# Performance work log

Hardware: AMD Instinct MI355X
Metric: run time of the kernel (lower is better)

## Reference

```python
import jax, jax.numpy as jnp
import numpy as np

B, N, IN, E, H, F = 64, 256, 128, 256, 8, 1024


def setup_inputs() -> dict:
    key = jax.random.key(0)
    ks = jax.random.split(key, 16)
    x = jax.random.normal(ks[0], (B, N, IN), jnp.float32)
    adj = (jax.random.uniform(ks[1], (B, N, N)) < 0.1).astype(jnp.float32)
    adj = jnp.maximum(adj, adj.transpose(0, 2, 1))  # symmetric 0/1 adjacency
    mask = jax.random.randint(ks[2], (B, N), 0, 2).astype(jnp.float32)
    dist = jax.random.normal(ks[3], (B, N, N), jnp.float32)

    def lin(k, i, o):
        return (jax.random.normal(k, (i, o), jnp.float32) / np.sqrt(i)).astype(jnp.float32)

    return dict(
        x=x, adj=adj, mask=mask, dist=dist,
        W1=lin(ks[4], IN, E), b1=jnp.zeros((E,), jnp.float32),
        W2=lin(ks[5], E, E), b2=jnp.zeros((E,), jnp.float32),
        W3=lin(ks[6], E, E), b3=jnp.zeros((E,), jnp.float32),
        ln1_g=jnp.ones((E,), jnp.float32), ln1_b=jnp.zeros((E,), jnp.float32),
        Wq=lin(ks[7], E, H * E), Wk=lin(ks[8], E, H * E), Wv=lin(ks[9], E, H * E),
        Wo=lin(ks[10], H * E, E), bo=jnp.zeros((E,), jnp.float32),
        ln2_g=jnp.ones((E,), jnp.float32), ln2_b=jnp.zeros((E,), jnp.float32),
        Wf1=lin(ks[11], E, F), bf1=jnp.zeros((F,), jnp.float32),
        Wf2=lin(ks[12], F, E), bf2=jnp.zeros((E,), jnp.float32),
    )


def _layernorm(x, g, b):
    m = x.mean(-1, keepdims=True)
    v = ((x - m) ** 2).mean(-1, keepdims=True)
    return (x - m) * jax.lax.rsqrt(v + 1e-5) * g + b


def reference(x, adj, mask, dist, W1, b1, W2, b2, W3, b3, ln1_g, ln1_b,
              Wq, Wk, Wv, Wo, bo, ln2_g, ln2_b, Wf1, bf1, Wf2, bf2):
    # --- DenseGCNConv normalization (add self-loops, sym-normalize) ---
    eye = jnp.eye(N, dtype=adj.dtype)
    A = adj * (1.0 - eye) + eye                      # fill_diag(adj, 1)
    dis = jax.lax.rsqrt(jnp.clip(A.sum(-1), 1.0, None))
    An = dis[:, :, None] * A * dis[:, None, :]       # D^-1/2 A D^-1/2, [B,N,N]
    m3 = mask[:, :, None]

    def gcn(h, W, b):
        return (jnp.einsum('bij,bjf->bif', An, h @ W) + b) * m3

    g1 = jax.nn.relu(gcn(x, W1, b1))
    g2 = jax.nn.relu(gcn(g1, W2, b2))
    g3 = jax.nn.relu(gcn(g2, W3, b3))
    gcn_res = g1 + g2 + g3

    # --- masked MHA with distance bias (head dim = E per head) ---
    h = _layernorm(gcn_res, ln1_g, ln1_b)
    mh = mask[:, None, :, None]                      # [B,1,N,1]
    q = (h @ Wq).reshape(B, N, H, E).transpose(0, 2, 1, 3) * mh
    k = (h @ Wk).reshape(B, N, H, E).transpose(0, 2, 1, 3) * mh
    v = (h @ Wv).reshape(B, N, H, E).transpose(0, 2, 1, 3) * mh
    a = jnp.einsum('bhne,bhme->bhnm', q * (E ** -0.5), k) + dist[:, None]
    am = (mask[:, :, None] * mask[:, None, :])[:, None]  # [B,1,N,N]
    a = jnp.where(am == 0, -1e9, a)
    a = jax.nn.softmax(a, axis=-1)
    a = jnp.where(am == 0, 0.0, a)
    y = jnp.einsum('bhnm,bhme->bhne', a, v).transpose(0, 2, 1, 3).reshape(B, N, H * E)
    y = (y @ Wo + bo) * m3
    att = gcn_res + y

    # --- FFN block ---
    f = _layernorm(att, ln2_g, ln2_b)
    f = (jax.nn.gelu(f @ Wf1 + bf1, approximate=False) @ Wf2 + bf2) * m3
    att = att + f
    return gcn_res + att
```

## Files before the change

### kernel.cpp

```cpp
#include <hip/hip_runtime.h>
#include <hip/hip_bf16.h>
#include <cmath>

#define BB 64
#define NNODES 256
#define INF_ 128
#define EE 256
#define HH 8
#define FFN 1024
#define BNROWS 16384

typedef __attribute__((ext_vector_type(8))) short short8;
typedef __attribute__((ext_vector_type(4))) float floatx4;
typedef __attribute__((ext_vector_type(4))) unsigned short ushort4v;

__device__ __forceinline__ float b2f(unsigned short u) {
  union { unsigned u32; float f; } w; w.u32 = ((unsigned)u) << 16; return w.f;
}
__device__ __forceinline__ unsigned short f2b(float f) {
  union { float f; unsigned u32; } w; w.f = f;
  unsigned r = w.u32 + 0x7FFFu + ((w.u32 >> 16) & 1u);
  return (unsigned short)(r >> 16);
}
__device__ __forceinline__ float gelu_f(float x) {
  const float z = 0.7978845608028654f * (x + 0.044715f * x * x * x);
  const float e = __expf(2.0f * z);
  const float th = (e - 1.0f) / (e + 1.0f);
  return 0.5f * x * (1.0f + th);
}

typedef const __attribute__((address_space(1))) void GV;
typedef __attribute__((address_space(3))) void LV;

__device__ __forceinline__ void gl_lds16(const unsigned short* g,
                                         unsigned short* l, int lane) {
#if __has_builtin(__builtin_amdgcn_global_load_lds)
  __builtin_amdgcn_global_load_lds((GV*)g, (LV*)l, 16, 0, 0);
#else
  *(short8*)(l + lane * 8) = *(const short8*)g;
#endif
}

struct PackArgs {
  const float* src[10];
  unsigned short* dst[10];
  int R[10], C[10];
  int start[11];
};

__launch_bounds__(256)
__global__ void pack_kernel(PackArgs a)
{
  __shared__ float tile[32][33];
  const int bid = blockIdx.x;
  int j = 0;
  while (bid >= a.start[j + 1]) j++;
  const int lb = bid - a.start[j];
  const float* src = a.src[j];
  unsigned short* dst = a.dst[j];
  const int R = a.R[j], C = a.C[j];

  if (C == 0) {
    const int i = (lb * 256 + threadIdx.x) * 4;
    if (i >= R) return;
    floatx4 v = *(const floatx4*)(src + i);
    ushort4v o;
    #pragma unroll
    for (int k = 0; k < 4; k++) o[k] = f2b(v[k]);
    *(ushort4v*)(dst + i) = o;
    return;
  }
  const int tpr = C >> 5;
  const int c0 = (lb % tpr) * 32, r0 = (lb / tpr) * 32;
  const int tx = threadIdx.x & 31, ty = threadIdx.x >> 5;
  #pragma unroll
  for (int i = ty; i < 32; i += 8)
    tile[i][tx] = src[(long long)(r0 + i) * C + c0 + tx];
  __syncthreads();
  #pragma unroll
  for (int i = ty; i < 32; i += 8)
    dst[(long long)(c0 + i) * R + r0 + tx] = f2b(tile[tx][i]);
}

__launch_bounds__(1024)
__global__ void an_kernel(const float* __restrict__ adj,
                          unsigned short* __restrict__ An)
{
  __shared__ float dis[256];
  const int b = blockIdx.x;
  const float* A = adj + (long long)b * 65536;
  const int t = threadIdx.x;
  const int row = t >> 2, seg = t & 3;
  const float* p = A + row * 256 + seg * 64;
  float s = 0.f;
  for (int k = 0; k < 64; k += 4) {
    floatx4 v = *(const floatx4*)(p + k);
    #pragma unroll
    for (int jj = 0; jj < 4; jj++) {
      const int col = seg * 64 + k + jj;
      s += (col == row) ? 1.0f : v[jj];
    }
  }
  s += __shfl_xor(s, 1);
  s += __shfl_xor(s, 2);
  if (seg == 0) dis[row] = 1.0f / sqrtf(fmaxf(s, 1.0f));
  __syncthreads();
  const float di = dis[row];
  unsigned short* dst = An + (long long)b * 65536 + row * 256 + seg * 64;
  for (int k = 0; k < 64; k += 4) {
    floatx4 v = *(const floatx4*)(p + k);
    ushort4v o;
    #pragma unroll
    for (int jj = 0; jj < 4; jj++) {
      const int col = seg * 64 + k + jj;
      o[jj] = f2b(di * dis[col] * ((col == row) ? 1.0f : v[jj]));
    }
    *(ushort4v*)(dst + k) = o;
  }
}

__launch_bounds__(512, 4)
__global__ void gemm_kernel(const unsigned short* __restrict__ A, int lda,
                            long long sAo, long long sAi,
                            const unsigned short* __restrict__ Bm, int ldb,
                            long long sBo, long long sBi,
                            void* __restrict__ Cv, int ldc,
                            long long sCo, long long sCi,
                            int K, int zshift, int mode, int flag,
                            const float* __restrict__ aux1,
                            const float* __restrict__ mask,
                            float* __restrict__ gcn,
                            void* __restrict__ aux2)
{
  __shared__ __align__(16) unsigned short sA[16384];
  __shared__ __align__(16) unsigned short sB[16384];

  const int t = threadIdx.x;
  const int z = blockIdx.z;
  const int zi = z & ((1 << zshift) - 1);
  const int zb = z >> zshift;
  const int m0 = blockIdx.x * 128;
  const int n0 = blockIdx.y * 128;
  A  += zb * sAo + zi * sAi;
  Bm += zb * sBo + zi * sBi;
  const long long cbase = zb * sCo + zi * sCi;

  const int lane = t & 63;
  const int w = t >> 6;
  const int wm = w >> 2, wn = w & 3;
  const int lm = lane & 15, qd = lane >> 4;

  floatx4 acc[4][2] = {};

  const int sub = lane >> 4;
  const int qs  = lane & 15;
  const unsigned short* pA[4];
  const unsigned short* pB[4];
  #pragma unroll
  for (int i = 0; i < 4; i++) {
    const int d = w * 4 + i;
    const int r = d * 4 + sub;
    const int co = (qs ^ (r & 7)) * 8;
    pA[i] = A + (long long)(m0 + r) * lda + co;
    pB[i] = Bm + (long long)(n0 + r) * ldb + co;
  }

  for (int kk = 0; kk < K; kk += 128) {
    #pragma unroll
    for (int i = 0; i < 4; i++) {
      gl_lds16(pA[i] + kk, &sA[(w * 4 + i) * 512], lane);
      gl_lds16(pB[i] + kk, &sB[(w * 4 + i) * 512], lane);
    }
    __syncthreads();

    #pragma unroll
    for (int ks = 0; ks < 4; ks++) {
      short8 af[4], bg[2];
      const int q = ks * 4 + qd;
      #pragma unroll
      for (int mi = 0; mi < 4; mi++) {
        const int r = wm * 64 + mi * 16 + lm;
        af[mi] = *(const short8*)&sA[r * 128 + ((q ^ (r & 7)) * 8)];
      }
      #pragma unroll
      for (int ni = 0; ni < 2; ni++) {
        const int r = wn * 32 + ni * 16 + lm;
        bg[ni] = *(const short8*)&sB[r * 128 + ((q ^ (r & 7)) * 8)];
      }
      #pragma unroll
      for (int mi = 0; mi < 4; mi++)
        #pragma unroll
        for (int ni = 0; ni < 2; ni++)
          acc[mi][ni] = __builtin_amdgcn_mfma_f32_16x16x32_bf16(
              af[mi], bg[ni], acc[mi][ni], 0, 0, 0);
    }
    __syncthreads();
  }

  #pragma unroll
  for (int mi = 0; mi < 4; mi++) {
    const int row0 = m0 + wm * 64 + mi * 16 + qd * 4;
    #pragma unroll
    for (int ni = 0; ni < 2; ni++) {
      const int col = n0 + wn * 32 + ni * 16 + lm;
      floatx4 a = acc[mi][ni];
      if (mode == 0) {
        float* Cf = (float*)Cv;
        #pragma unroll
        for (int r = 0; r < 4; r++)
          Cf[cbase + (long long)(row0 + r) * ldc + col] = a[r];
      } else if (mode == 1) {
        unsigned short* Cb = (unsigned short*)Cv;
        #pragma unroll
        for (int r = 0; r < 4; r++)
          Cb[cbase + (long long)(row0 + r) * ldc + col] = f2b(a[r]);
      } else if (mode == 2) {
        float* Cf = (float*)Cv;
        #pragma unroll
        for (int r = 0; r < 4; r++)
          Cf[cbase + (long long)(row0 + r) * ldc + col] += a[r];
      } else if (mode == 3) {
        unsigned short* Cb = (unsigned short*)Cv;
        const float bv = aux1[col];
        #pragma unroll
        for (int r = 0; r < 4; r++)
          Cb[cbase + (long long)(row0 + r) * ldc + col] = f2b(gelu_f(a[r] + bv));
      } else if (mode == 5) {
        const int b = row0 >> 8, n = row0 & 255;
        ushort4v o;
        #pragma unroll
        for (int r = 0; r < 4; r++) o[r] = f2b(a[r]);
        *(ushort4v*)((unsigned short*)Cv + (long long)b * 65536 + col * 256 + n) = o;
      } else if (mode == 8) {
        float* Cf = (float*)Cv;
        const float* attf = (const float*)aux2;
        const float bv = aux1[col];
        #pragma unroll
        for (int r = 0; r < 4; r++) {
          const long long idx = (long long)(row0 + r) * 256 + col;
          Cf[idx] = gcn[idx] + attf[idx] + (a[r] + bv) * mask[row0 + r];
        }
      } else if (mode == 9) {
        const int token = zb * 256 + col;
        const float m = mask[token];
        ushort4v o; floatx4 g;
        #pragma unroll
        for (int r = 0; r < 4; r++) {
          const float v = fmaxf((a[r] + aux1[row0 + r]) * m, 0.f);
          o[r] = f2b(v); g[r] = v;
        }
        *(ushort4v*)((unsigned short*)Cv + (long long)token * 256 + row0) = o;
        float* gp = gcn + (long long)token * 256 + row0;
        if (flag) { floatx4 old = *(const floatx4*)gp; g += old; }
        *(floatx4*)gp = g;
      } else if (mode == 12) {
        float* Cf = (float*)Cv;
        const float bv = aux1[col];
        #pragma unroll
        for (int r = 0; r < 4; r++) {
          const long long idx = (long long)(row0 + r) * 256 + col;
          Cf[idx] = gcn[idx] + (a[r] + bv) * mask[row0 + r];
        }
      } else if (mode == 13) {
        unsigned short* Cb = (unsigned short*)Cv;
        #pragma unroll
        for (int r = 0; r < 4; r++)
          Cb[cbase + (long long)(row0 + r) * ldc + col] = f2b(a[r] * 0.0625f);
      } else {
        const int z2 = (row0 >> 8) * 8 + (col >> 8);
        const int e = col & 255, n = row0 & 255;
        ushort4v o;
        #pragma unroll
        for (int r = 0; r < 4; r++) o[r] = f2b(a[r]);
        *(ushort4v*)((unsigned short*)Cv + (long long)z2 * 65536 + e * 256 + n) = o;
      }
    }
  }
}

__launch_bounds__(512, 2)
__global__ void attn_kernel(const unsigned short* __restrict__ HBF,
                            const unsigned short* __restrict__ ABH,
                            const unsigned short* __restrict__ VT,
                            unsigned short* __restrict__ YB,
                            const float* __restrict__ dist,
                            const float* __restrict__ mask)
{
  __shared__ __align__(16) unsigned short sA8[8192];
  __shared__ __align__(16) unsigned short sB16[16384];
  __shared__ float redm[4][128];
  __shared__ float reds[4][128];

  const int mt = blockIdx.x;
  const int z  = blockIdx.y;
  const int b  = z >> 3, h = z & 7;
  const int t = threadIdx.x, lane = t & 63, w = t >> 6;
  const int wm = w >> 2, wn = w & 3;
  const int lm = lane & 15, qd = lane >> 4;
  const int m0 = mt * 128;

  const unsigned short* Hm = HBF + ((long long)(b * 256 + m0)) * 256;
  const unsigned short* Hb = HBF + ((long long)(b * 256)) * 256;
  const unsigned short* AB = ABH + (long long)h * 65536;
  const unsigned short* Vb = VT + (long long)z * 65536;
  unsigned short* Yb = YB + ((long long)(b * 256 + m0)) * 2048 + h * 256;
  const float* maskb = mask + b * 256;
  const float* distb = dist + (long long)b * 65536;

  const int rin = lane >> 3;
  const int qs  = lane & 7;

  floatx4 T[4][4] = {};
  for (int c = 0; c < 4; c++) {
    const int e0 = c * 64;
    #pragma unroll
    for (int i = 0; i < 2; i++) {
      const int d = w * 2 + i;
      const int r = d * 8 + rin;
      gl_lds16(Hm + (long long)r * 256 + e0 + ((qs ^ (r & 7)) * 8),
               &sA8[d * 512], lane);
    }
    #pragma unroll
    for (int i = 0; i < 4; i++) {
      const int d = w * 4 + i;
      const int r = d * 8 + rin;
      gl_lds16(AB + (long long)r * 256 + e0 + ((qs ^ (r & 7)) * 8),
               &sB16[d * 512], lane);
    }
    __syncthreads();
    #pragma unroll
    for (int ks = 0; ks < 2; ks++) {
      short8 af[4], bg4[4];
      const int o = ks * 4 + qd;
      #pragma unroll
      for (int mi = 0; mi < 4; mi++) {
        const int r = wm * 64 + mi * 16 + lm;
        af[mi] = *(const short8*)&sA8[r * 64 + ((o ^ (r & 7)) * 8)];
      }
      #pragma unroll
      for (int ni = 0; ni < 4; ni++) {
        const int r = wn * 64 + ni * 16 + lm;
        bg4[ni] = *(const short8*)&sB16[r * 64 + ((o ^ (r & 7)) * 8)];
      }
      #pragma unroll
      for (int mi = 0; mi < 4; mi++)
        #pragma unroll
        for (int ni = 0; ni < 4; ni++)
          T[mi][ni] = __builtin_amdgcn_mfma_f32_16x16x32_bf16(
              af[mi], bg4[ni], T[mi][ni], 0, 0, 0);
    }
    __syncthreads();
  }

  floatx4 S[4][4] = {};
  for (int c = 0; c < 4; c++) {
    #pragma unroll
    for (int i = 0; i < 4; i++) {
      const int d = w * 4 + i;
      const int r = d * 8 + rin;
      gl_lds16(Hb + (long long)r * 256 + c * 64 + ((qs ^ (r & 7)) * 8),
               &sB16[d * 512], lane);
    }
    if (wn == c) {
      #pragma unroll
      for (int mi = 0; mi < 4; mi++)
        #pragma unroll
        for (int r = 0; r < 4; r++) {
          const int row = wm * 64 + mi * 16 + qd * 4 + r;
          #pragma unroll
          for (int ni = 0; ni < 4; ni++) {
            const int kl = ni * 16 + lm;
            const int slot = (kl >> 3) ^ (row & 7);
            sA8[row * 64 + slot * 8 + (kl & 7)] = f2b(T[mi][ni][r]);
          }
        }
    }
    __syncthreads();
    #pragma unroll
    for (int ks = 0; ks < 2; ks++) {
      short8 af[4], bg4[4];
      const int o = ks * 4 + qd;
      #pragma unroll
      for (int mi = 0; mi < 4; mi++) {
        const int r = wm * 64 + mi * 16 + lm;
        af[mi] = *(const short8*)&sA8[r * 64 + ((o ^ (r & 7)) * 8)];
      }
      #pragma unroll
      for (int ni = 0; ni < 4; ni++) {
        const int r = wn * 64 + ni * 16 + lm;
        bg4[ni] = *(const short8*)&sB16[r * 64 + ((o ^ (r & 7)) * 8)];
      }
      #pragma unroll
      for (int mi = 0; mi < 4; mi++)
        #pragma unroll
        for (int ni = 0; ni < 4; ni++)
          S[mi][ni] = __builtin_amdgcn_mfma_f32_16x16x32_bf16(
              af[mi], bg4[ni], S[mi][ni], 0, 0, 0);
    }
    __syncthreads();
  }

  #pragma unroll
  for (int i = 0; i < 4; i++) {
    const int d = w * 4 + i;
    const int r = d * 8 + rin;
    gl_lds16(Vb + (long long)r * 256 + ((qs ^ (r & 7)) * 8),
             &sB16[d * 512], lane);
  }

  float mk[4];
  #pragma unroll
  for (int ni = 0; ni < 4; ni++) mk[ni] = maskb[wn * 64 + ni * 16 + lm];

  float lred[4][4];
  #pragma unroll
  for (int mi = 0; mi < 4; mi++) {
    #pragma unroll
    for (int r = 0; r < 4; r++) {
      const int row = wm * 64 + mi * 16 + qd * 4 + r;
      const float mq = maskb[m0 + row];
      float mx = -3e38f;
      #pragma unroll
      for (int ni = 0; ni < 4; ni++) {
        const int col = wn * 64 + ni * 16 + lm;
        const float dv = distb[(long long)(m0 + row) * 256 + col];
        const float v = (mq != 0.f && mk[ni] != 0.f) ? (S[mi][ni][r] + dv) : -1e9f;
        S[mi][ni][r] = v;
        mx = fmaxf(mx, v);
      }
      lred[mi][r] = mx;
    }
  }
  #pragma unroll
  for (int off = 1; off < 16; off <<= 1)
    #pragma unroll
    for (int mi = 0; mi < 4; mi++)
      #pragma unroll
      for (int r = 0; r < 4; r++)
        lred[mi][r] = fmaxf(lred[mi][r], __shfl_xor(lred[mi][r], off));
  if (lm == 0)
    #pragma unroll
    for (int mi = 0; mi < 4; mi++)
      #pragma unroll
      for (int r = 0; r < 4; r++)
        redm[wn][wm * 64 + mi * 16 + qd * 4 + r] = lred[mi][r];
  __syncthreads();

  #pragma unroll
  for (int mi = 0; mi < 4; mi++) {
    #pragma unroll
    for (int r = 0; r < 4; r++) {
      const int row = wm * 64 + mi * 16 + qd * 4 + r;
      const float gmax = fmaxf(fmaxf(redm[0][row], redm[1][row]),
                               fmaxf(redm[2][row], redm[3][row]));
      float s = 0.f;
      #pragma unroll
      for (int ni = 0; ni < 4; ni++) {
        const float e = __expf(S[mi][ni][r] - gmax);
        S[mi][ni][r] = e;
        s += e;
      }
      lred[mi][r] = s;
    }
  }
  #pragma unroll
  for (int off = 1; off < 16; off <<= 1)
    #pragma unroll
    for (int mi = 0; mi < 4; mi++)
      #pragma unroll
      for (int r = 0; r < 4; r++)
        lred[mi][r] += __shfl_xor(lred[mi][r], off);
  if (lm == 0)
    #pragma unroll
    for (int mi = 0; mi < 4; mi++)
      #pragma unroll
      for (int r = 0; r < 4; r++)
        reds[wn][wm * 64 + mi * 16 + qd * 4 + r] = lred[mi][r];
  __syncthreads();

  #pragma unroll
  for (int mi = 0; mi < 4; mi++) {
    #pragma unroll
    for (int r = 0; r < 4; r++) {
      const int row = wm * 64 + mi * 16 + qd * 4 + r;
      const float gs = reds[0][row] + reds[1][row] + reds[2][row] + reds[3][row];
      const float inv = 1.0f / gs;
      #pragma unroll
      for (int ni = 0; ni < 4; ni++) S[mi][ni][r] *= inv;
    }
  }

  floatx4 Y[4][4] = {};
  for (int c = 0; c < 4; c++) {
    if (wn == c) {
      #pragma unroll
      for (int mi = 0; mi < 4; mi++)
        #pragma unroll
        for (int r = 0; r < 4; r++) {
          const int row = wm * 64 + mi * 16 + qd * 4 + r;
          #pragma unroll
          for (int ni = 0; ni < 4; ni++) {
            const int kl = ni * 16 + lm;
            const int slot = (kl >> 3) ^ (row & 7);
            sA8[row * 64 + slot * 8 + (kl & 7)] = f2b(S[mi][ni][r]);
          }
        }
    }
    __syncthreads();
    #pragma unroll
    for (int ks = 0; ks < 2; ks++) {
      short8 af[4], bg4[4];
      const int o = ks * 4 + qd;
      #pragma unroll
      for (int mi = 0; mi < 4; mi++) {
        const int r = wm * 64 + mi * 16 + lm;
        af[mi] = *(const short8*)&sA8[r * 64 + ((o ^ (r & 7)) * 8)];
      }
      #pragma unroll
      for (int ni = 0; ni < 4; ni++) {
        const int r = wn * 64 + ni * 16 + lm;
        bg4[ni] = *(const short8*)&sB16[r * 64 + ((o ^ (r & 7)) * 8)];
      }
      #pragma unroll
      for (int mi = 0; mi < 4; mi++)
        #pragma unroll
        for (int ni = 0; ni < 4; ni++)
          Y[mi][ni] = __builtin_amdgcn_mfma_f32_16x16x32_bf16(
              af[mi], bg4[ni], Y[mi][ni], 0, 0, 0);
    }
    __syncthreads();
    if (c < 3) {
      #pragma unroll
      for (int i = 0; i < 4; i++) {
        const int d = w * 4 + i;
        const int r = d * 8 + rin;
        gl_lds16(Vb + (long long)r * 256 + (c + 1) * 64 + ((qs ^ (r & 7)) * 8),
                 &sB16[d * 512], lane);
      }
    }
  }

  #pragma unroll
  for (int mi = 0; mi < 4; mi++)
    #pragma unroll
    for (int ni = 0; ni < 4; ni++) {
      const int col = wn * 64 + ni * 16 + lm;
      #pragma unroll
      for (int r = 0; r < 4; r++) {
        const int row = wm * 64 + mi * 16 + qd * 4 + r;
        Yb[(long long)row * 2048 + col] = f2b(Y[mi][ni][r]);
      }
    }
}

__global__ void ln_kernel(const float* __restrict__ X,
                          const float* __restrict__ gam,
                          const float* __restrict__ bet,
                          unsigned short* __restrict__ out)
{
  const int g = blockIdx.x * 4 + (threadIdx.x >> 6);
  const int lane = threadIdx.x & 63;
  floatx4 v = *(const floatx4*)(X + (long long)g * 256 + lane * 4);
  float s = v[0] + v[1] + v[2] + v[3];
  float sq = v[0]*v[0] + v[1]*v[1] + v[2]*v[2] + v[3]*v[3];
  #pragma unroll
  for (int off = 32; off > 0; off >>= 1) {
    s  += __shfl_xor(s, off);
    sq += __shfl_xor(sq, off);
  }
  const float mean = s * (1.0f / 256.0f);
  const float var = sq * (1.0f / 256.0f) - mean * mean;
  const float rs = 1.0f / sqrtf(var + 1e-5f);
  ushort4v o;
  #pragma unroll
  for (int jj = 0; jj < 4; jj++) {
    const int c = lane * 4 + jj;
    o[jj] = f2b((v[jj] - mean) * rs * gam[c] + bet[c]);
  }
  *(ushort4v*)(out + (long long)g * 256 + lane * 4) = o;
}

static inline void launch_gemm(hipStream_t st, int M, int N, int batch,
    const void* A, int lda, long long sAo, long long sAi,
    const void* B, int ldb, long long sBo, long long sBi,
    void* C, int ldc, long long sCo, long long sCi,
    int K, int zshift, int mode, int flag,
    const float* aux1, const float* mask, float* gcn, void* aux2)
{
  dim3 grid(M / 128, N / 128, batch), blk(512);
  gemm_kernel<<<grid, blk, 0, st>>>(
      (const unsigned short*)A, lda, sAo, sAi,
      (const unsigned short*)B, ldb, sBo, sBi,
      C, ldc, sCo, sCi, K, zshift, mode, flag, aux1, mask, gcn, aux2);
}

extern "C" void kernel_launch(void* const* d_in, const int* in_sizes, int n_in,
                              void* d_out, int out_size, void* d_ws, size_t ws_size,
                              hipStream_t stream)
{
  (void)in_sizes; (void)n_in; (void)out_size;
  const float* x    = (const float*)d_in[0];
  const float* adj  = (const float*)d_in[1];
  const float* mask = (const float*)d_in[2];
  const float* dist = (const float*)d_in[3];
  const float* W1   = (const float*)d_in[4];
  const float* b1   = (const float*)d_in[5];
  const float* W2   = (const float*)d_in[6];
  const float* b2   = (const float*)d_in[7];
  const float* W3   = (const float*)d_in[8];
  const float* b3   = (const float*)d_in[9];
  const float* ln1g = (const float*)d_in[10];
  const float* ln1b = (const float*)d_in[11];
  const float* Wq   = (const float*)d_in[12];
  const float* Wk   = (const float*)d_in[13];
  const float* Wv   = (const float*)d_in[14];
  const float* Wo   = (const float*)d_in[15];
  const float* bo   = (const float*)d_in[16];
  const float* ln2g = (const float*)d_in[17];
  const float* ln2b = (const float*)d_in[18];
  const float* Wf1  = (const float*)d_in[19];
  const float* bf1  = (const float*)d_in[20];
  const float* Wf2  = (const float*)d_in[21];
  const float* bf2  = (const float*)d_in[22];

  char* w = (char*)d_ws;
  auto alloc = [&](size_t sz) { void* p = (void*)w; w += sz; return p; };
  unsigned short* W1T   = (unsigned short*)alloc(65536);
  unsigned short* W2T   = (unsigned short*)alloc(131072);
  unsigned short* W3T   = (unsigned short*)alloc(131072);
  unsigned short* WVT   = (unsigned short*)alloc(1048576);
  unsigned short* WOT   = (unsigned short*)alloc(1048576);
  unsigned short* WF1T  = (unsigned short*)alloc(524288);
  unsigned short* WF2T  = (unsigned short*)alloc(524288);
  unsigned short* WQb   = (unsigned short*)alloc(1048576);
  unsigned short* WKb   = (unsigned short*)alloc(1048576);
  unsigned short* ABH   = (unsigned short*)alloc(1048576);
  unsigned short* XBF   = (unsigned short*)alloc(4194304);
  float*          GCN   = (float*)         alloc(16777216);
  float*          U     = (float*)         alloc(16777216);
  unsigned short* HBF   = (unsigned short*)alloc(8388608);
  char* scratch = (char*)alloc(134217728);
  if ((size_t)(w - (char*)d_ws) > ws_size) return;
  unsigned short* AN  = (unsigned short*)scratch;
  unsigned short* TT  = (unsigned short*)(scratch + 8388608);
  unsigned short* GBF = (unsigned short*)(scratch + 16777216);
  unsigned short* VT  = (unsigned short*)scratch;
  unsigned short* YB  = (unsigned short*)(scratch + 67108864);
  unsigned short* FFB = (unsigned short*)scratch;

  PackArgs pa;
  const float* srcs[10] = {W1, W2, W3, Wv, Wo, Wf1, Wf2, x, Wq, Wk};
  unsigned short* dsts[10] = {W1T, W2T, W3T, WVT, WOT, WF1T, WF2T, XBF, WQb, WKb};
  const int Rs[10] = {128, 256, 256, 256, 2048, 256, 1024,
                      BNROWS * INF_, EE * HH * EE, EE * HH * EE};
  const int Cs[10] = {256, 256, 256, 2048, 256, 1024, 256, 0, 0, 0};
  const int sts[11] = {0, 32, 96, 160, 672, 1184, 1440, 1696, 3744, 4256, 4768};
  for (int j = 0; j < 10; j++) {
    pa.src[j] = srcs[j]; pa.dst[j] = dsts[j]; pa.R[j] = Rs[j]; pa.C[j] = Cs[j];
  }
  for (int j = 0; j < 11; j++) pa.start[j] = sts[j];
  pack_kernel<<<4768, 256, 0, stream>>>(pa);

  an_kernel<<<64, 1024, 0, stream>>>(adj, AN);

  launch_gemm(stream, 256, 256, 8, WKb, 2048, 256, 0, WQb, 2048, 256, 0,
              ABH, 256, 65536, 0, 256, 0, 13, 0, nullptr, nullptr, nullptr, nullptr);

  launch_gemm(stream, BNROWS, EE, 1, XBF, 128, 0,0, W1T, 128, 0,0,
              TT, 256, 0,0, 128, 0, 5, 0, nullptr, nullptr, nullptr, nullptr);
  launch_gemm(stream, 256, 256, BB, TT, 256, 65536,0, AN, 256, 65536,0,
              GBF, 256, 0,0, 256, 0, 9, 0, b1, mask, GCN, nullptr);
  launch_gemm(stream, BNROWS, EE, 1, GBF, 256, 0,0, W2T, 256, 0,0,
              TT, 256, 0,0, 256, 0, 5, 0, nullptr, nullptr, nullptr, nullptr);
  launch_gemm(stream, 256, 256, BB, TT, 256, 65536,0, AN, 256, 65536,0,
              GBF, 256, 0,0, 256, 0, 9, 1, b2, mask, GCN, nullptr);
  launch_gemm(stream, BNROWS, EE, 1, GBF, 0x100, 0,0, W3T, 256, 0,0,
              TT, 256, 0,0, 256, 0, 5, 0, nullptr, nullptr, nullptr, nullptr);
  launch_gemm(stream, 256, 256, BB, TT, 256, 65536,0, AN, 256, 65536,0,
              GBF, 256, 0,0, 256, 0, 9, 1, b3, mask, GCN, nullptr);

  ln_kernel<<<4096, 256, 0, stream>>>(GCN, ln1g, ln1b, HBF);

  launch_gemm(stream, BNROWS, 2048, 1, HBF, 256, 0,0, WVT, 256, 0,0,
              VT, 0, 0,0, 256, 0, 14, 0, nullptr, nullptr, nullptr, nullptr);
  attn_kernel<<<dim3(2, 512), 512, 0, stream>>>(HBF, ABH, VT, YB, dist, mask);
  launch_gemm(stream, BNROWS, EE, 1, YB, 2048, 0,0, WOT, 2048, 0,0,
              U, 256, 0,0, 2048, 0, 12, 0, bo, mask, GCN, nullptr);

  ln_kernel<<<4096, 256, 0, stream>>>(U, ln2g, ln2b, HBF);
  launch_gemm(stream, BNROWS, FFN, 1, HBF, 256, 0,0, WF1T, 256, 0,0,
              FFB, 1024, 0,0, 256, 0, 3, 0, bf1, nullptr, nullptr, nullptr);
  launch_gemm(stream, BNROWS, EE, 1, FFB, 1024, 0,0, WF2T, 1024, 0,0,
              d_out, 256, 0,0, 1024, 0, 8, 0, bf2, mask, GCN, U);
}
```

Measured before the change: 528.8 us.

## Precompute Q·K-projected rows in one wide GEMM and read bf16 dist

Attention previously computed T = H·(Wq Wk^T) per tile inside the attention kernel before the score GEMM. It now computes that projection for all rows together with V in a single 4096-column GEMM over HBF, with ABH and WVT placed adjacent. The attention kernel loads the precomputed projection and reuses the same buffer for its output. The distance bias is also converted once to bf16 in the pack kernel, halving its read traffic. In exchange the code adds an extra intermediate write and read, more pack work, bf16 rounding on dist, and relies on the ABH/WVT contiguity.

```diff
diff --git a/kernel.cpp b/kernel.cpp
--- a/kernel.cpp
+++ b/kernel.cpp
@@ -42,10 +42,10 @@
 }
 
 struct PackArgs {
-  const float* src[10];
-  unsigned short* dst[10];
-  int R[10], C[10];
-  int start[11];
+  const float* src[12];
+  unsigned short* dst[12];
+  int R[12], C[12];
+  int start[13];
 };
 
 __launch_bounds__(256)
@@ -267,23 +267,29 @@
         for (int r = 0; r < 4; r++)
           Cb[cbase + (long long)(row0 + r) * ldc + col] = f2b(a[r] * 0.0625f);
       } else {
-        const int z2 = (row0 >> 8) * 8 + (col >> 8);
-        const int e = col & 255, n = row0 & 255;
-        ushort4v o;
-        #pragma unroll
-        for (int r = 0; r < 4; r++) o[r] = f2b(a[r]);
-        *(ushort4v*)((unsigned short*)Cv + (long long)z2 * 65536 + e * 256 + n) = o;
+        if (col < 2048) {
+          unsigned short* Cb = (unsigned short*)Cv;
+          #pragma unroll
+          for (int r = 0; r < 4; r++)
+            Cb[(long long)(row0 + r) * 2048 + col] = f2b(a[r]);
+        } else {
+          const int z2 = (row0 >> 8) * 8 + ((col >> 8) - 8);
+          const int e = col & 255, n = row0 & 255;
+          ushort4v o;
+          #pragma unroll
+          for (int r = 0; r < 4; r++) o[r] = f2b(a[r]);
+          *(ushort4v*)((unsigned short*)aux2 + (long long)z2 * 65536 + e * 256 + n) = o;
+        }
       }
     }
   }
 }
 
 __launch_bounds__(512, 2)
-__global__ void attn_kernel(const unsigned short* __restrict__ HBF,
-                            const unsigned short* __restrict__ ABH,
+__global__ void attn_kernel(unsigned short* __restrict__ QP,
+                            const unsigned short* __restrict__ HBF,
                             const unsigned short* __restrict__ VT,
-                            unsigned short* __restrict__ YB,
-                            const float* __restrict__ dist,
+                            const unsigned short* __restrict__ DSTB,
                             const float* __restrict__ mask)
 {
   __shared__ __align__(16) unsigned short sA8[8192];
@@ -299,81 +305,31 @@
   const int lm = lane & 15, qd = lane >> 4;
   const int m0 = mt * 128;
 
-  const unsigned short* Hm = HBF + ((long long)(b * 256 + m0)) * 256;
-  const unsigned short* Hb = HBF + ((long long)(b * 256)) * 256;
-  const unsigned short* AB = ABH + (long long)h * 65536;
+  unsigned short* Qm = QP + ((long long)(b * 256 + m0)) * 2048 + h * 256;
+  const unsigned short* Hb = HBF + ((long long)b) * 65536;
   const unsigned short* Vb = VT + (long long)z * 65536;
-  unsigned short* Yb = YB + ((long long)(b * 256 + m0)) * 2048 + h * 256;
+  const unsigned short* db = DSTB + (long long)b * 65536;
   const float* maskb = mask + b * 256;
-  const float* distb = dist + (long long)b * 65536;
 
   const int rin = lane >> 3;
   const int qs  = lane & 7;
 
-  floatx4 T[4][4] = {};
+  floatx4 S[4][4] = {};
   for (int c = 0; c < 4; c++) {
     const int e0 = c * 64;
     #pragma unroll
     for (int i = 0; i < 2; i++) {
       const int d = w * 2 + i;
       const int r = d * 8 + rin;
-      gl_lds16(Hm + (long long)r * 256 + e0 + ((qs ^ (r & 7)) * 8),
+      gl_lds16(Qm + (long long)r * 2048 + e0 + ((qs ^ (r & 7)) * 8),
                &sA8[d * 512], lane);
     }
     #pragma unroll
     for (int i = 0; i < 4; i++) {
       const int d = w * 4 + i;
       const int r = d * 8 + rin;
-      gl_lds16(AB + (long long)r * 256 + e0 + ((qs ^ (r & 7)) * 8),
+      gl_lds16(Hb + (long long)r * 256 + e0 + ((qs ^ (r & 7)) * 8),
                &sB16[d * 512], lane);
-    }
-    __syncthreads();
-    #pragma unroll
-    for (int ks = 0; ks < 2; ks++) {
-      short8 af[4], bg4[4];
-      const int o = ks * 4 + qd;
-      #pragma unroll
-      for (int mi = 0; mi < 4; mi++) {
-        const int r = wm * 64 + mi * 16 + lm;
-        af[mi] = *(const short8*)&sA8[r * 64 + ((o ^ (r & 7)) * 8)];
-      }
-      #pragma unroll
-      for (int ni = 0; ni < 4; ni++) {
-        const int r = wn * 64 + ni * 16 + lm;
-        bg4[ni] = *(const short8*)&sB16[r * 64 + ((o ^ (r & 7)) * 8)];
-      }
-      #pragma unroll
-      for (int mi = 0; mi < 4; mi++)
-        #pragma unroll
-        for (int ni = 0; ni < 4; ni++)
-          T[mi][ni] = __builtin_amdgcn_mfma_f32_16x16x32_bf16(
-              af[mi], bg4[ni], T[mi][ni], 0, 0, 0);
-    }
-    __syncthreads();
-  }
-
-  floatx4 S[4][4] = {};
-  for (int c = 0; c < 4; c++) {
-    #pragma unroll
-    for (int i = 0; i < 4; i++) {
-      const int d = w * 4 + i;
-      const int r = d * 8 + rin;
-      gl_lds16(Hb + (long long)r * 256 + c * 64 + ((qs ^ (r & 7)) * 8),
-               &sB16[d * 512], lane);
-    }
-    if (wn == c) {
-      #pragma unroll
-      for (int mi = 0; mi < 4; mi++)
-        #pragma unroll
-        for (int r = 0; r < 4; r++) {
-          const int row = wm * 64 + mi * 16 + qd * 4 + r;
-          #pragma unroll
-          for (int ni = 0; ni < 4; ni++) {
-            const int kl = ni * 16 + lm;
-            const int slot = (kl >> 3) ^ (row & 7);
-            sA8[row * 64 + slot * 8 + (kl & 7)] = f2b(T[mi][ni][r]);
-          }
-        }
     }
     __syncthreads();
     #pragma unroll
@@ -423,7 +379,7 @@
       #pragma unroll
       for (int ni = 0; ni < 4; ni++) {
         const int col = wn * 64 + ni * 16 + lm;
-        const float dv = distb[(long long)(m0 + row) * 256 + col];
+        const float dv = b2f(db[(long long)(m0 + row) * 256 + col]);
         const float v = (mq != 0.f && mk[ni] != 0.f) ? (S[mi][ni][r] + dv) : -1e9f;
         S[mi][ni][r] = v;
         mx = fmaxf(mx, v);
@@ -548,7 +504,7 @@
       #pragma unroll
       for (int r = 0; r < 4; r++) {
         const int row = wm * 64 + mi * 16 + qd * 4 + r;
-        Yb[(long long)row * 2048 + col] = f2b(Y[mi][ni][r]);
+        Qm[(long long)row * 2048 + col] = f2b(Y[mi][ni][r]);
       }
     }
 }
@@ -628,14 +584,15 @@
   unsigned short* W1T   = (unsigned short*)alloc(65536);
   unsigned short* W2T   = (unsigned short*)alloc(131072);
   unsigned short* W3T   = (unsigned short*)alloc(131072);
+  unsigned short* ABH   = (unsigned short*)alloc(1048576);
   unsigned short* WVT   = (unsigned short*)alloc(1048576);
   unsigned short* WOT   = (unsigned short*)alloc(1048576);
   unsigned short* WF1T  = (unsigned short*)alloc(524288);
   unsigned short* WF2T  = (unsigned short*)alloc(524288);
   unsigned short* WQb   = (unsigned short*)alloc(1048576);
   unsigned short* WKb   = (unsigned short*)alloc(1048576);
-  unsigned short* ABH   = (unsigned short*)alloc(1048576);
   unsigned short* XBF   = (unsigned short*)alloc(4194304);
+  unsigned short* DSTB  = (unsigned short*)alloc(8388608);
   float*          GCN   = (float*)         alloc(16777216);
   float*          U     = (float*)         alloc(16777216);
   unsigned short* HBF   = (unsigned short*)alloc(8388608);
@@ -644,22 +601,22 @@
   unsigned short* AN  = (unsigned short*)scratch;
   unsigned short* TT  = (unsigned short*)(scratch + 8388608);
   unsigned short* GBF = (unsigned short*)(scratch + 16777216);
-  unsigned short* VT  = (unsigned short*)scratch;
-  unsigned short* YB  = (unsigned short*)(scratch + 67108864);
+  unsigned short* QPB = (unsigned short*)scratch;
+  unsigned short* VT  = (unsigned short*)(scratch + 67108864);
   unsigned short* FFB = (unsigned short*)scratch;
 
   PackArgs pa;
-  const float* srcs[10] = {W1, W2, W3, Wv, Wo, Wf1, Wf2, x, Wq, Wk};
-  unsigned short* dsts[10] = {W1T, W2T, W3T, WVT, WOT, WF1T, WF2T, XBF, WQb, WKb};
-  const int Rs[10] = {128, 256, 256, 256, 2048, 256, 1024,
-                      BNROWS * INF_, EE * HH * EE, EE * HH * EE};
-  const int Cs[10] = {256, 256, 256, 2048, 256, 1024, 256, 0, 0, 0};
-  const int sts[11] = {0, 32, 96, 160, 672, 1184, 1440, 1696, 3744, 4256, 4768};
-  for (int j = 0; j < 10; j++) {
+  const float* srcs[11] = {W1, W2, W3, Wv, Wo, Wf1, Wf2, x, Wq, Wk, dist};
+  unsigned short* dsts[11] = {W1T, W2T, W3T, WVT, WOT, WF1T, WF2T, XBF, WQb, WKb, DSTB};
+  const int Rs[11] = {128, 256, 256, 256, 2048, 256, 1024,
+                      BNROWS * INF_, EE * HH * EE, EE * HH * EE, BB * 65536};
+  const int Cs[11] = {256, 256, 256, 2048, 256, 1024, 256, 0, 0, 0, 0};
+  const int sts[12] = {0, 32, 96, 160, 672, 1184, 1440, 1696, 3744, 4256, 4768, 8864};
+  for (int j = 0; j < 11; j++) {
     pa.src[j] = srcs[j]; pa.dst[j] = dsts[j]; pa.R[j] = Rs[j]; pa.C[j] = Cs[j];
   }
-  for (int j = 0; j < 11; j++) pa.start[j] = sts[j];
-  pack_kernel<<<4768, 256, 0, stream>>>(pa);
+  for (int j = 0; j < 12; j++) pa.start[j] = sts[j];
+  pack_kernel<<<8864, 256, 0, stream>>>(pa);
 
   an_kernel<<<64, 1024, 0, stream>>>(adj, AN);
 
@@ -674,17 +631,17 @@
               TT, 256, 0,0, 256, 0, 5, 0, nullptr, nullptr, nullptr, nullptr);
   launch_gemm(stream, 256, 256, BB, TT, 256, 65536,0, AN, 256, 65536,0,
               GBF, 256, 0,0, 256, 0, 9, 1, b2, mask, GCN, nullptr);
-  launch_gemm(stream, BNROWS, EE, 1, GBF, 0x100, 0,0, W3T, 256, 0,0,
+  launch_gemm(stream, BNROWS, EE, 1, GBF, 256, 0,0, W3T, 256, 0,0,
               TT, 256, 0,0, 256, 0, 5, 0, nullptr, nullptr, nullptr, nullptr);
   launch_gemm(stream, 256, 256, BB, TT, 256, 65536,0, AN, 256, 65536,0,
               GBF, 256, 0,0, 256, 0, 9, 1, b3, mask, GCN, nullptr);
 
   ln_kernel<<<4096, 256, 0, stream>>>(GCN, ln1g, ln1b, HBF);
 
-  launch_gemm(stream, BNROWS, 2048, 1, HBF, 256, 0,0, WVT, 256, 0,0,
-              VT, 0, 0,0, 256, 0, 14, 0, nullptr, nullptr, nullptr, nullptr);
-  attn_kernel<<<dim3(2, 512), 512, 0, stream>>>(HBF, ABH, VT, YB, dist, mask);
-  launch_gemm(stream, BNROWS, EE, 1, YB, 2048, 0,0, WOT, 2048, 0,0,
+  launch_gemm(stream, BNROWS, 4096, 1, HBF, 256, 0,0, ABH, 256, 0,0,
+              QPB, 2048, 0,0, 256, 0, 15, 0, nullptr, nullptr, nullptr, VT);
+  attn_kernel<<<dim3(2, 512), 512, 0, stream>>>(QPB, HBF, VT, DSTB, mask);
+  launch_gemm(stream, BNROWS, EE, 1, QPB, 2048, 0,0, WOT, 2048, 0,0,
               U, 256, 0,0, 2048, 0, 12, 0, bo, mask, GCN, nullptr);
 
   ln_kernel<<<4096, 256, 0, stream>>>(U, ln2g, ln2b, HBF);
```

After: 520.0 us. About the same (-1.7%).
